# Optimization experiments

Measured on AMD Instinct MI355X. Metric: run time of the kernel, lower is better.

Reference implementation:

```python
import jax, jax.numpy as jnp
import numpy as np
from jax import lax

# --- configuration matching init_kwargs ---
N = 512          # head_size: square cost matrices, marginals a=b=ones(N)
REG = 0.05       # entropy_reg
TAU = 1000.0     # absorption threshold on scaling vectors
N_ITER = 50      # max_iter (fixed iteration count; tol early-exit omitted)
BATCH = 128


def setup_inputs() -> dict:
    key = jax.random.key(0)
    # nonnegative cost matrices, uniform [0,1)
    X = jax.random.uniform(key, (BATCH, N, N), dtype=jnp.float32)
    return {"X": X}


def _sinkhorn_stabilized(M):
    """Log-stabilized Sinkhorn (POT sinkhorn_stabilized) for one cost matrix M [N,N].

    Marginals a = b = ones(N). Returns transport plan Gamma [N,N].
    """
    a = jnp.ones((N,), M.dtype)
    b = jnp.ones((N,), M.dtype)

    def step(carry, _):
        alpha, beta, u, v = carry
        # K = exp(-(M - alpha_i - beta_j)/reg)
        K = jnp.exp((alpha[:, None] + beta[None, :] - M) / REG)
        v = b / (K.T @ u)
        u = a / (K @ v)
        # tau-based absorption of large scalings into the log-domain potentials
        absorb = (jnp.max(jnp.abs(u)) > TAU) | (jnp.max(jnp.abs(v)) > TAU)
        alpha = jnp.where(absorb, alpha + REG * jnp.log(u), alpha)
        beta = jnp.where(absorb, beta + REG * jnp.log(v), beta)
        u = jnp.where(absorb, jnp.full_like(u, 1.0 / N), u)
        v = jnp.where(absorb, jnp.full_like(v, 1.0 / N), v)
        return (alpha, beta, u, v), None

    init = (
        jnp.zeros((N,), M.dtype),          # alpha
        jnp.zeros((N,), M.dtype),          # beta
        jnp.full((N,), 1.0 / N, M.dtype),  # u
        jnp.full((N,), 1.0 / N, M.dtype),  # v
    )
    (alpha, beta, u, v), _ = lax.scan(step, init, None, length=N_ITER)
    # Gamma = exp(-(M - alpha_i - beta_j)/reg + log u_i + log v_j)
    Gamma = jnp.exp(
        (alpha[:, None] + beta[None, :] - M) / REG
        + jnp.log(u)[:, None]
        + jnp.log(v)[None, :]
    )
    return Gamma


def reference(X):
    # original mutates X[i] in place per batch element; we return the batched result
    return jax.vmap(_sinkhorn_stabilized)(X)
```

## Files before the change

kernel.cpp:

```cpp
#include <hip/hip_runtime.h>

constexpr int BN = 512;
constexpr int NITER = 50;

#define CEXP  (-28.853900817779268f)
#define ESH   (14.0f)
#define L2TAU (9.965784284662087f)

typedef unsigned int u32;

__device__ __forceinline__ float fexp2(float x) { return __builtin_amdgcn_exp2f(x); }
__device__ __forceinline__ float flog2(float x) { return __builtin_amdgcn_logf(x); }

__device__ __forceinline__ float nr_rcp(float x) {
    float r = __builtin_amdgcn_rcpf(x);
    return fmaf(r, fmaf(-x, r, 1.0f), r);
}

template <int CTRL>
__device__ __forceinline__ float dppx(float x) {
    return __int_as_float(__builtin_amdgcn_update_dpp(
        0, __float_as_int(x), CTRL, 0xF, 0xF, true));
}

__device__ __forceinline__ float bfly_sum(float x) {
    x += dppx<0xB1>(x);
    x += dppx<0x4E>(x);
    x += dppx<0x141>(x);
    x += dppx<0x140>(x);
    x += __shfl_xor(x, 16, 64);
    x += __shfl_xor(x, 32, 64);
    return x;
}
__device__ __forceinline__ float bfly_max(float x) {
    x = fmaxf(x, dppx<0xB1>(x));
    x = fmaxf(x, dppx<0x4E>(x));
    x = fmaxf(x, dppx<0x141>(x));
    x = fmaxf(x, dppx<0x140>(x));
    x = fmaxf(x, __shfl_xor(x, 16, 64));
    x = fmaxf(x, __shfl_xor(x, 32, 64));
    return x;
}

__device__ __forceinline__ void fma_mix2(float& accLo, float& accHi, u32 e2,
                                         float pLo, float pHi) {
    asm("v_fma_mix_f32 %0, %2, %3, %0 op_sel_hi:[1,0,0]\n\t"
        "v_fma_mix_f32 %1, %2, %4, %1 op_sel:[1,0,0] op_sel_hi:[1,0,0]"
        : "+v"(accLo), "+v"(accHi)
        : "v"(e2), "v"(pLo), "v"(pHi));
}

__device__ __forceinline__ void barrier_lgkm() {
    asm volatile("s_waitcnt lgkmcnt(0)\n\ts_barrier" ::: "memory");
}

__global__ __launch_bounds__(256)
void prep_exp_t(const float* __restrict__ X, float* __restrict__ out)
{
    const int blk  = blockIdx.x;
    const int b    = blk >> 4;
    const int tile = blk & 15;
    const int i0   = (tile >> 2) << 7;
    const int j0   = (tile & 3) << 7;
    const int tid  = threadIdx.x;

    const float* __restrict__ Mb = X + (size_t)b * (BN * BN);
    _Float16* __restrict__ Et = reinterpret_cast<_Float16*>(out + (size_t)b * (BN * BN));

    __shared__ _Float16 T[128][130];

    #pragma unroll
    for (int k = 0; k < 16; ++k) {
        int idx = tid + (k << 8);
        int fi  = idx >> 5;
        int fj  = idx & 31;
        float4 m = *reinterpret_cast<const float4*>(Mb + (size_t)(i0 + fi) * BN + j0 + (fj << 2));
        T[(fj << 2) + 0][fi] = (_Float16)fexp2(fmaf(m.x, CEXP, ESH));
        T[(fj << 2) + 1][fi] = (_Float16)fexp2(fmaf(m.y, CEXP, ESH));
        T[(fj << 2) + 2][fi] = (_Float16)fexp2(fmaf(m.z, CEXP, ESH));
        T[(fj << 2) + 3][fi] = (_Float16)fexp2(fmaf(m.w, CEXP, ESH));
    }
    __syncthreads();
    #pragma unroll
    for (int k = 0; k < 32; ++k) {
        int o  = tid + (k << 8);
        int j  = o >> 6;
        int c2 = o & 63;
        u32 val = *reinterpret_cast<const u32*>(&T[j][c2 << 1]);
        *reinterpret_cast<u32*>(Et + (size_t)(j0 + j) * BN + i0 + (c2 << 1)) = val;
    }
}

__device__ __forceinline__ void consume4(
    uint4 c0, uint4 c1, uint4 c2, uint4 c3, int jb,
    float pr0, float pr1, float pr2, float pr3,
    float pr4, float pr5, float pr6, float pr7,
    float& a0, float& a1, float& a2, float& a3,
    float& a4, float& a5, float& a6, float& a7,
    float& vml, const float* bh, float* lv, int lane)
{
    const float4 bh4 = *reinterpret_cast<const float4*>(&bh[jb]);

    float s00 = 0.f, s01 = 0.f;
    fma_mix2(s00, s01, c0.x, pr0, pr1); fma_mix2(s00, s01, c0.y, pr2, pr3);
    fma_mix2(s00, s01, c0.z, pr4, pr5); fma_mix2(s00, s01, c0.w, pr6, pr7);
    float s10 = 0.f, s11 = 0.f;
    fma_mix2(s10, s11, c1.x, pr0, pr1); fma_mix2(s10, s11, c1.y, pr2, pr3);
    fma_mix2(s10, s11, c1.z, pr4, pr5); fma_mix2(s10, s11, c1.w, pr6, pr7);
    float s20 = 0.f, s21 = 0.f;
    fma_mix2(s20, s21, c2.x, pr0, pr1); fma_mix2(s20, s21, c2.y, pr2, pr3);
    fma_mix2(s20, s21, c2.z, pr4, pr5); fma_mix2(s20, s21, c2.w, pr6, pr7);
    float s30 = 0.f, s31 = 0.f;
    fma_mix2(s30, s31, c3.x, pr0, pr1); fma_mix2(s30, s31, c3.y, pr2, pr3);
    fma_mix2(s30, s31, c3.z, pr4, pr5); fma_mix2(s30, s31, c3.w, pr6, pr7);

    float r0 = bfly_sum(s00 + s01);
    float r1 = bfly_sum(s10 + s11);
    float r2 = bfly_sum(s20 + s21);
    float r3 = bfly_sum(s30 + s31);

    float t0 = r0 * 0x1p-14f, t1 = r1 * 0x1p-14f;
    float t2 = r2 * 0x1p-14f, t3 = r3 * 0x1p-14f;
    float q0 = nr_rcp(t0), q1 = nr_rcp(t1), q2 = nr_rcp(t2), q3 = nr_rcp(t3);
    float l0 = -bh4.x - flog2(t0), l1 = -bh4.y - flog2(t1);
    float l2 = -bh4.z - flog2(t2), l3 = -bh4.w - flog2(t3);
    vml = fmaxf(vml, fmaxf(fmaxf(l0, l1), fmaxf(l2, l3)));
    if (lane == 0)
        *reinterpret_cast<float4*>(&lv[jb]) = make_float4(l0, l1, l2, l3);

    fma_mix2(a0, a1, c0.x, q0, q0); fma_mix2(a2, a3, c0.y, q0, q0);
    fma_mix2(a4, a5, c0.z, q0, q0); fma_mix2(a6, a7, c0.w, q0, q0);
    fma_mix2(a0, a1, c1.x, q1, q1); fma_mix2(a2, a3, c1.y, q1, q1);
    fma_mix2(a4, a5, c1.z, q1, q1); fma_mix2(a6, a7, c1.w, q1, q1);
    fma_mix2(a0, a1, c2.x, q2, q2); fma_mix2(a2, a3, c2.y, q2, q2);
    fma_mix2(a4, a5, c2.z, q2, q2); fma_mix2(a6, a7, c2.w, q2, q2);
    fma_mix2(a0, a1, c3.x, q3, q3); fma_mix2(a2, a3, c3.y, q3, q3);
    fma_mix2(a4, a5, c3.z, q3, q3); fma_mix2(a6, a7, c3.w, q3, q3);
}

__global__ __launch_bounds__(1024)
__attribute__((amdgpu_waves_per_eu(4, 4)))
void sinkhorn_w1024(const float* __restrict__ X, float* __restrict__ out,
                    float* __restrict__ cucv)
{
    const int b    = blockIdx.x;
    const int t    = threadIdx.x;
    const int lane = t & 63;
    const int w    = t >> 6;

    const u32* __restrict__ Et4 =
        reinterpret_cast<const u32*>(out + (size_t)b * (BN * BN));

    __shared__ float ah[BN], bh[BN], lu[BN], lv[BN], pv[BN];
    __shared__ float tpart[8][BN];
    __shared__ float wmaxlu[16], wmaxlv[16];
    __shared__ uint4 stage[16][8][64];

    if (t < BN) {
        ah[t] = 0.f; bh[t] = 0.f;
        lu[t] = -9.f; lv[t] = -9.f;
        pv[t] = 0x1p-9f;
    }

    const int jb0 = w << 5;
    const u32* gbase = Et4 + (size_t)jb0 * 256 + (lane << 2);
#define LD(c) (*reinterpret_cast<const uint4*>(gbase + (size_t)(c) * 256))

    #pragma unroll
    for (int c = 0; c < 8; ++c)
        stage[w][c][lane] = LD(24 + c);

    uint4 e0 = LD(0), e1 = LD(1), e2 = LD(2), e3 = LD(3);
    uint4 f0 = LD(4), f1 = LD(5), f2 = LD(6), f3 = LD(7);
    uint4 h0, h1, h2, h3;

    __syncthreads();

    for (int it = 0; it < NITER; ++it) {
        const float4 prA = *reinterpret_cast<const float4*>(&pv[lane * 8]);
        const float4 prB = *reinterpret_cast<const float4*>(&pv[lane * 8 + 4]);
        const float pr0 = prA.x, pr1 = prA.y, pr2 = prA.z, pr3 = prA.w;
        const float pr4 = prB.x, pr5 = prB.y, pr6 = prB.z, pr7 = prB.w;

        float a0 = 0.f, a1 = 0.f, a2 = 0.f, a3 = 0.f;
        float a4 = 0.f, a5 = 0.f, a6 = 0.f, a7 = 0.f;
        float vml = -1e30f;

#define STEP(B0,B1,B2,B3, I0,I1,I2,I3, ICOL, JOFF)                            \
        I0 = LD((ICOL) + 0); I1 = LD((ICOL) + 1);                             \
        I2 = LD((ICOL) + 2); I3 = LD((ICOL) + 3);                             \
        consume4(B0, B1, B2, B3, jb0 + (JOFF),                                \
                 pr0, pr1, pr2, pr3, pr4, pr5, pr6, pr7,                      \
                 a0, a1, a2, a3, a4, a5, a6, a7, vml, bh, lv, lane);

        STEP(e0,e1,e2,e3, h0,h1,h2,h3,  8,  0)
        STEP(f0,f1,f2,f3, e0,e1,e2,e3, 12,  4)
        STEP(h0,h1,h2,h3, f0,f1,f2,f3, 16,  8)
        STEP(e0,e1,e2,e3, h0,h1,h2,h3, 20, 12)
        STEP(f0,f1,f2,f3, e0,e1,e2,e3,  0, 16)
        STEP(h0,h1,h2,h3, f0,f1,f2,f3,  4, 20)
#undef STEP

        #pragma unroll
        for (int ls = 0; ls < 2; ++ls) {
            uint4 l0v = stage[w][ls * 4 + 0][lane];
            uint4 l1v = stage[w][ls * 4 + 1][lane];
            uint4 l2v = stage[w][ls * 4 + 2][lane];
            uint4 l3v = stage[w][ls * 4 + 3][lane];
            consume4(l0v, l1v, l2v, l3v, jb0 + 24 + ls * 4,
                     pr0, pr1, pr2, pr3, pr4, pr5, pr6, pr7,
                     a0, a1, a2, a3, a4, a5, a6, a7, vml, bh, lv, lane);
        }

        if (w < 8) {
            *reinterpret_cast<float4*>(&tpart[w][lane * 8]) = make_float4(a0, a1, a2, a3);
            *reinterpret_cast<float4*>(&tpart[w][lane * 8 + 4]) = make_float4(a4, a5, a6, a7);
        }
        if (lane == 0) wmaxlv[w] = vml;
        barrier_lgkm();
        if (w >= 8) {
            float4* p0 = reinterpret_cast<float4*>(&tpart[w - 8][lane * 8]);
            float4* p1 = reinterpret_cast<float4*>(&tpart[w - 8][lane * 8 + 4]);
            float4 o0 = *p0, o1 = *p1;
            o0.x += a0; o0.y += a1; o0.z += a2; o0.w += a3;
            o1.x += a4; o1.y += a5; o1.z += a6; o1.w += a7;
            *p0 = o0; *p1 = o1;
        }
        barrier_lgkm();

        float lun = 0.f, tt = 0.f;
        if (t < BN) {
            float p0 = 0, p1 = 0, p2 = 0, p3 = 0;
            #pragma unroll
            for (int w2 = 0; w2 < 8; w2 += 4) {
                p0 += tpart[w2 + 0][t];
                p1 += tpart[w2 + 1][t];
                p2 += tpart[w2 + 2][t];
                p3 += tpart[w2 + 3][t];
            }
            tt  = ((p0 + p1) + (p2 + p3)) * 0x1p-14f;
            lun = -ah[t] - flog2(tt);
            float m = bfly_max(lun);
            if (lane == 0) wmaxlu[w] = m;
        }
        barrier_lgkm();

        if (t < BN) {
            float mlu = wmaxlu[0], mlv = wmaxlv[0];
            #pragma unroll
            for (int i2 = 1; i2 < 8; ++i2)  mlu = fmaxf(mlu, wmaxlu[i2]);
            #pragma unroll
            for (int i2 = 1; i2 < 16; ++i2) mlv = fmaxf(mlv, wmaxlv[i2]);
            if (mlu > L2TAU || mlv > L2TAU) {
                float an = ah[t] + lun;
                ah[t] = an;
                lu[t] = -9.f;
                pv[t] = fexp2(an - 9.0f);
                bh[t] += lv[t];
                lv[t] = -9.f;
            } else {
                lu[t] = lun;
                pv[t] = nr_rcp(tt);
            }
        }
        barrier_lgkm();
    }
#undef LD

    if (t < BN) {
        cucv[(size_t)b * 1024 + t]       = ah[t] + lu[t];
        cucv[(size_t)b * 1024 + 512 + t] = bh[t] + lv[t];
    }
}

__global__ __launch_bounds__(512)
__attribute__((amdgpu_waves_per_eu(2, 2)))
void sinkhorn_w512(const float* __restrict__ X, float* __restrict__ out,
                   float* __restrict__ cucv)
{
    const int b    = blockIdx.x;
    const int t    = threadIdx.x;
    const int lane = t & 63;
    const int w    = t >> 6;

    const u32* __restrict__ Et4 =
        reinterpret_cast<const u32*>(out + (size_t)b * (BN * BN));

    __shared__ float ah[BN], bh[BN], lu[BN], lv[BN], pv[BN];
    __shared__ float tpart[8][BN];
    __shared__ float wmaxlu[8], wmaxlv[8];
    __shared__ uint4 stage[8][16][64];

    ah[t] = 0.f; bh[t] = 0.f;
    lu[t] = -9.f; lv[t] = -9.f;
    pv[t] = 0x1p-9f;

    const int jb0 = w << 6;
    const u32* gbase = Et4 + (size_t)jb0 * 256 + (lane << 2);
#define LD(c) (*reinterpret_cast<const uint4*>(gbase + (size_t)(c) * 256))

    #pragma unroll
    for (int c = 0; c < 16; ++c)
        stage[w][c][lane] = LD(48 + c);

    uint4 e0 = LD(0),  e1 = LD(1),  e2 = LD(2),  e3 = LD(3);
    uint4 f0 = LD(4),  f1 = LD(5),  f2 = LD(6),  f3 = LD(7);
    uint4 h0 = LD(8),  h1 = LD(9),  h2 = LD(10), h3 = LD(11);
    uint4 k0, k1, k2, k3;

    __syncthreads();

    for (int it = 0; it < NITER; ++it) {
        const float4 prA = *reinterpret_cast<const float4*>(&pv[lane * 8]);
        const float4 prB = *reinterpret_cast<const float4*>(&pv[lane * 8 + 4]);
        const float pr0 = prA.x, pr1 = prA.y, pr2 = prA.z, pr3 = prA.w;
        const float pr4 = prB.x, pr5 = prB.y, pr6 = prB.z, pr7 = prB.w;

        float a0 = 0.f, a1 = 0.f, a2 = 0.f, a3 = 0.f;
        float a4 = 0.f, a5 = 0.f, a6 = 0.f, a7 = 0.f;
        float vml = -1e30f;

#define STEP(B0,B1,B2,B3, I0,I1,I2,I3, ICOL, JOFF)                            \
        I0 = LD((ICOL) + 0); I1 = LD((ICOL) + 1);                             \
        I2 = LD((ICOL) + 2); I3 = LD((ICOL) + 3);                             \
        consume4(B0, B1, B2, B3, jb0 + (JOFF),                                \
                 pr0, pr1, pr2, pr3, pr4, pr5, pr6, pr7,                      \
                 a0, a1, a2, a3, a4, a5, a6, a7, vml, bh, lv, lane);

        STEP(e0,e1,e2,e3, k0,k1,k2,k3, 12,  0)
        STEP(f0,f1,f2,f3, e0,e1,e2,e3, 16,  4)
        STEP(h0,h1,h2,h3, f0,f1,f2,f3, 20,  8)
        STEP(k0,k1,k2,k3, h0,h1,h2,h3, 24, 12)
        STEP(e0,e1,e2,e3, k0,k1,k2,k3, 28, 16)
        STEP(f0,f1,f2,f3, e0,e1,e2,e3, 32, 20)
        STEP(h0,h1,h2,h3, f0,f1,f2,f3, 36, 24)
        STEP(k0,k1,k2,k3, h0,h1,h2,h3, 40, 28)
        STEP(e0,e1,e2,e3, k0,k1,k2,k3, 44, 32)
        STEP(f0,f1,f2,f3, e0,e1,e2,e3,  0, 36)
        STEP(h0,h1,h2,h3, f0,f1,f2,f3,  4, 40)
        STEP(k0,k1,k2,k3, h0,h1,h2,h3,  8, 44)
#undef STEP

        #pragma unroll
        for (int ls = 0; ls < 4; ++ls) {
            uint4 l0v = stage[w][ls * 4 + 0][lane];
            uint4 l1v = stage[w][ls * 4 + 1][lane];
            uint4 l2v = stage[w][ls * 4 + 2][lane];
            uint4 l3v = stage[w][ls * 4 + 3][lane];
            consume4(l0v, l1v, l2v, l3v, jb0 + 48 + ls * 4,
                     pr0, pr1, pr2, pr3, pr4, pr5, pr6, pr7,
                     a0, a1, a2, a3, a4, a5, a6, a7, vml, bh, lv, lane);
        }

        *reinterpret_cast<float4*>(&tpart[w][lane * 8]) = make_float4(a0, a1, a2, a3);
        *reinterpret_cast<float4*>(&tpart[w][lane * 8 + 4]) = make_float4(a4, a5, a6, a7);
        if (lane == 0) wmaxlv[w] = vml;
        barrier_lgkm();

        float p0 = 0, p1 = 0, p2 = 0, p3 = 0;
        #pragma unroll
        for (int w2 = 0; w2 < 8; w2 += 4) {
            p0 += tpart[w2 + 0][t];
            p1 += tpart[w2 + 1][t];
            p2 += tpart[w2 + 2][t];
            p3 += tpart[w2 + 3][t];
        }
        float tt  = ((p0 + p1) + (p2 + p3)) * 0x1p-14f;
        float lun = -ah[t] - flog2(tt);
        float m = bfly_max(lun);
        if (lane == 0) wmaxlu[w] = m;
        barrier_lgkm();

        float mlu = wmaxlu[0], mlv = wmaxlv[0];
        #pragma unroll
        for (int i2 = 1; i2 < 8; ++i2) {
            mlu = fmaxf(mlu, wmaxlu[i2]);
            mlv = fmaxf(mlv, wmaxlv[i2]);
        }
        if (mlu > L2TAU || mlv > L2TAU) {
            float an = ah[t] + lun;
            ah[t] = an;
            lu[t] = -9.f;
            pv[t] = fexp2(an - 9.0f);
            bh[t] += lv[t];
            lv[t] = -9.f;
        } else {
            lu[t] = lun;
            pv[t] = nr_rcp(tt);
        }
        barrier_lgkm();
    }
#undef LD

    cucv[(size_t)b * 1024 + t]       = ah[t] + lu[t];
    cucv[(size_t)b * 1024 + 512 + t] = bh[t] + lv[t];
}

__global__ __launch_bounds__(256)
void gamma_out(const float* __restrict__ X, float* __restrict__ out,
               const float* __restrict__ cucv)
{
    const int blk  = blockIdx.x;
    const int b    = blk >> 4;
    const int tile = blk & 15;
    const int tid  = threadIdx.x;
    const int i0   = tile << 5;

    __shared__ float cu[32];
    __shared__ float cv[BN];

    if (tid < 32) cu[tid] = cucv[(size_t)b * 1024 + i0 + tid];
    cv[tid]        = cucv[(size_t)b * 1024 + 512 + tid];
    cv[tid + 256]  = cucv[(size_t)b * 1024 + 768 + tid];
    __syncthreads();

    const float* __restrict__ Mb = X + (size_t)b * (BN * BN);
    float* __restrict__ Gb = out + (size_t)b * (BN * BN);
    const float4* __restrict__ cv4 = reinterpret_cast<const float4*>(cv);

    #pragma unroll
    for (int k = 0; k < 16; ++k) {
        int idx = tid + (k << 8);
        int r   = idx >> 7;
        int c4  = idx & 127;
        int i   = i0 + r;
        float4 m = *reinterpret_cast<const float4*>(Mb + (size_t)i * BN + (c4 << 2));
        float4 c = cv4[c4];
        float cui = cu[r];
        float4 g;
        g.x = fexp2(fmaf(m.x, CEXP, cui + c.x));
        g.y = fexp2(fmaf(m.y, CEXP, cui + c.y));
        g.z = fexp2(fmaf(m.z, CEXP, cui + c.z));
        g.w = fexp2(fmaf(m.w, CEXP, cui + c.w));
        *reinterpret_cast<float4*>(Gb + (size_t)i * BN + (c4 << 2)) = g;
    }
}

extern "C" void kernel_launch(void* const* d_in, const int* in_sizes, int n_in,
                              void* d_out, int out_size, void* d_ws, size_t ws_size,
                              hipStream_t stream)
{
    const float* X = (const float*)d_in[0];
    float* out = (float*)d_out;
    const int batch = in_sizes[0] / (BN * BN);

    prep_exp_t<<<batch * 16, 256, 0, stream>>>(X, out);

    bool w1024_ok = false;
    hipFuncAttributes fa{};
    if (hipFuncGetAttributes(&fa, (const void*)sinkhorn_w1024) == hipSuccess)
        w1024_ok = (fa.localSizeBytes == 0 && fa.numRegs >= 96);

    const size_t cucv_bytes = (size_t)batch * 1024 * sizeof(float);
    if (ws_size >= cucv_bytes) {
        float* cucv = (float*)d_ws;
        if (w1024_ok)
            sinkhorn_w1024<<<batch, 1024, 0, stream>>>(X, out, cucv);
        else
            sinkhorn_w512<<<batch, 512, 0, stream>>>(X, out, cucv);
        gamma_out<<<batch * 16, 256, 0, stream>>>(X, out, cucv);
    } else {
        float* cucv = (float*)d_ws;
        sinkhorn_w512<<<batch, 512, 0, stream>>>(X, out, cucv);
        gamma_out<<<batch * 16, 256, 0, stream>>>(X, out, cucv);
    }
}
```

Measured before the change: 646.7 us.

## Replace log-domain Sinkhorn with scaling-domain v2 kernel using permlane swaps

Adds a new 512-thread Sinkhorn kernel that keeps potentials and scalings in the multiplicative domain, using reciprocals and products instead of per-element log2 and exp2. The tau absorption check becomes a comparison on scaled values, and an extra barrier runs only when absorption fires. Each wave now handles 64 columns with a deeper register/LDS prefetch ring. Cross-half wave reductions use permlane16/32 swap builtins where available instead of shuffles. The 1024-thread kernel is removed. This trades the transcendental work and an extra barrier round for higher register and LDS pressure per wave, and for precision risk from raw rcp without Newton refinement and from the multiplicative potentials.

```diff
diff --git a/kernel.cpp b/kernel.cpp
--- a/kernel.cpp
+++ b/kernel.cpp
@@ -6,14 +6,17 @@
 #define CEXP  (-28.853900817779268f)
 #define ESH   (14.0f)
 #define L2TAU (9.965784284662087f)
+#define TAU_U (1000.0f)
+#define TAU_V (0.06103515625f)
 
 typedef unsigned int u32;
 
 __device__ __forceinline__ float fexp2(float x) { return __builtin_amdgcn_exp2f(x); }
 __device__ __forceinline__ float flog2(float x) { return __builtin_amdgcn_logf(x); }
+__device__ __forceinline__ float frcp(float x)  { return __builtin_amdgcn_rcpf(x); }
 
 __device__ __forceinline__ float nr_rcp(float x) {
-    float r = __builtin_amdgcn_rcpf(x);
+    float r = frcp(x);
     return fmaf(r, fmaf(-x, r, 1.0f), r);
 }
 
@@ -23,7 +26,59 @@
         0, __float_as_int(x), CTRL, 0xF, 0xF, true));
 }
 
+__device__ __forceinline__ float xadd16(float x) {
+#if __has_builtin(__builtin_amdgcn_permlane16_swap)
+    auto r = __builtin_amdgcn_permlane16_swap(__float_as_uint(x), __float_as_uint(x), false, false);
+    return __uint_as_float(r[0]) + __uint_as_float(r[1]);
+#else
+    return x + __shfl_xor(x, 16, 64);
+#endif
+}
+__device__ __forceinline__ float xadd32(float x) {
+#if __has_builtin(__builtin_amdgcn_permlane32_swap)
+    auto r = __builtin_amdgcn_permlane32_swap(__float_as_uint(x), __float_as_uint(x), false, false);
+    return __uint_as_float(r[0]) + __uint_as_float(r[1]);
+#else
+    return x + __shfl_xor(x, 32, 64);
+#endif
+}
+__device__ __forceinline__ float xmax16(float x) {
+#if __has_builtin(__builtin_amdgcn_permlane16_swap)
+    auto r = __builtin_amdgcn_permlane16_swap(__float_as_uint(x), __float_as_uint(x), false, false);
+    return fmaxf(__uint_as_float(r[0]), __uint_as_float(r[1]));
+#else
+    return fmaxf(x, __shfl_xor(x, 16, 64));
+#endif
+}
+__device__ __forceinline__ float xmax32(float x) {
+#if __has_builtin(__builtin_amdgcn_permlane32_swap)
+    auto r = __builtin_amdgcn_permlane32_swap(__float_as_uint(x), __float_as_uint(x), false, false);
+    return fmaxf(__uint_as_float(r[0]), __uint_as_float(r[1]));
+#else
+    return fmaxf(x, __shfl_xor(x, 32, 64));
+#endif
+}
+
 __device__ __forceinline__ float bfly_sum(float x) {
+    x += dppx<0xB1>(x);
+    x += dppx<0x4E>(x);
+    x += dppx<0x141>(x);
+    x += dppx<0x140>(x);
+    x = xadd16(x);
+    x = xadd32(x);
+    return x;
+}
+__device__ __forceinline__ float bfly_max(float x) {
+    x = fmaxf(x, dppx<0xB1>(x));
+    x = fmaxf(x, dppx<0x4E>(x));
+    x = fmaxf(x, dppx<0x141>(x));
+    x = fmaxf(x, dppx<0x140>(x));
+    x = xmax16(x);
+    x = xmax32(x);
+    return x;
+}
+
+__device__ __forceinline__ float bfly_sum_s(float x) {
     x += dppx<0xB1>(x);
     x += dppx<0x4E>(x);
     x += dppx<0x141>(x);
@@ -32,7 +87,7 @@
     x += __shfl_xor(x, 32, 64);
     return x;
 }
-__device__ __forceinline__ float bfly_max(float x) {
+__device__ __forceinline__ float bfly_max_s(float x) {
     x = fmaxf(x, dppx<0xB1>(x));
     x = fmaxf(x, dppx<0x4E>(x));
     x = fmaxf(x, dppx<0x141>(x));
@@ -91,15 +146,15 @@
     }
 }
 
-__device__ __forceinline__ void consume4(
+__device__ __forceinline__ void consume4v2(
     uint4 c0, uint4 c1, uint4 c2, uint4 c3, int jb,
     float pr0, float pr1, float pr2, float pr3,
     float pr4, float pr5, float pr6, float pr7,
     float& a0, float& a1, float& a2, float& a3,
     float& a4, float& a5, float& a6, float& a7,
-    float& vml, const float* bh, float* lv, int lane)
-{
-    const float4 bh4 = *reinterpret_cast<const float4*>(&bh[jb]);
+    float& vml, const float* pbh, float* qv, int lane)
+{
+    const float4 pb4 = *reinterpret_cast<const float4*>(&pbh[jb]);
 
     float s00 = 0.f, s01 = 0.f;
     fma_mix2(s00, s01, c0.x, pr0, pr1); fma_mix2(s00, s01, c0.y, pr2, pr3);
@@ -119,6 +174,172 @@
     float r2 = bfly_sum(s20 + s21);
     float r3 = bfly_sum(s30 + s31);
 
+    float q0 = frcp(r0), q1 = frcp(r1), q2 = frcp(r2), q3 = frcp(r3);
+
+    vml = fmaxf(vml, fmaxf(fmaxf(pb4.x * q0, pb4.y * q1),
+                           fmaxf(pb4.z * q2, pb4.w * q3)));
+    if (lane == 0)
+        *reinterpret_cast<float4*>(&qv[jb]) = make_float4(q0, q1, q2, q3);
+
+    fma_mix2(a0, a1, c0.x, q0, q0); fma_mix2(a2, a3, c0.y, q0, q0);
+    fma_mix2(a4, a5, c0.z, q0, q0); fma_mix2(a6, a7, c0.w, q0, q0);
+    fma_mix2(a0, a1, c1.x, q1, q1); fma_mix2(a2, a3, c1.y, q1, q1);
+    fma_mix2(a4, a5, c1.z, q1, q1); fma_mix2(a6, a7, c1.w, q1, q1);
+    fma_mix2(a0, a1, c2.x, q2, q2); fma_mix2(a2, a3, c2.y, q2, q2);
+    fma_mix2(a4, a5, c2.z, q2, q2); fma_mix2(a6, a7, c2.w, q2, q2);
+    fma_mix2(a0, a1, c3.x, q3, q3); fma_mix2(a2, a3, c3.y, q3, q3);
+    fma_mix2(a4, a5, c3.z, q3, q3); fma_mix2(a6, a7, c3.w, q3, q3);
+}
+
+__global__ __launch_bounds__(512)
+__attribute__((amdgpu_waves_per_eu(2, 2)))
+void sinkhorn_v2(const float* __restrict__ X, float* __restrict__ out,
+                 float* __restrict__ cucv)
+{
+    const int b    = blockIdx.x;
+    const int t    = threadIdx.x;
+    const int lane = t & 63;
+    const int w    = t >> 6;
+
+    const u32* __restrict__ Et4 =
+        reinterpret_cast<const u32*>(out + (size_t)b * (BN * BN));
+
+    __shared__ float pah[BN], pbh[BN], pv[BN], qv[BN];
+    __shared__ float tpart[8][BN];
+    __shared__ float wmaxlu[8], wmaxlv[2][8];
+    __shared__ uint4 stage[8][16][64];
+
+    pah[t] = 1.0f; pbh[t] = 1.0f;
+    pv[t]  = 0x1p-9f; qv[t] = 0x1p-9f;
+
+    const int jb0 = w << 6;
+    const u32* gbase = Et4 + (size_t)jb0 * 256 + (lane << 2);
+#define LD(c) (*reinterpret_cast<const uint4*>(gbase + (size_t)(c) * 256))
+
+    #pragma unroll
+    for (int c = 0; c < 16; ++c)
+        stage[w][c][lane] = LD(48 + c);
+
+    uint4 A0 = LD(0),  A1 = LD(1),  A2 = LD(2),  A3 = LD(3);
+    uint4 B0 = LD(4),  B1 = LD(5),  B2 = LD(6),  B3 = LD(7);
+    uint4 C0 = LD(8),  C1 = LD(9),  C2 = LD(10), C3 = LD(11);
+    uint4 D0 = LD(12), D1 = LD(13), D2 = LD(14), D3 = LD(15);
+    uint4 E0, E1, E2, E3, F0, F1, F2, F3;
+
+    __syncthreads();
+
+    for (int it = 0; it < NITER; ++it) {
+        const float4 prA = *reinterpret_cast<const float4*>(&pv[lane * 8]);
+        const float4 prB = *reinterpret_cast<const float4*>(&pv[lane * 8 + 4]);
+        const float pr0 = prA.x, pr1 = prA.y, pr2 = prA.z, pr3 = prA.w;
+        const float pr4 = prB.x, pr5 = prB.y, pr6 = prB.z, pr7 = prB.w;
+
+        float a0 = 0.f, a1 = 0.f, a2 = 0.f, a3 = 0.f;
+        float a4 = 0.f, a5 = 0.f, a6 = 0.f, a7 = 0.f;
+        float vml = 0.0f;
+
+#define STEP(P0,P1,P2,P3, N0,N1,N2,N3, ICOL, JOFF)                            \
+        N0 = LD((ICOL) + 0); N1 = LD((ICOL) + 1);                             \
+        N2 = LD((ICOL) + 2); N3 = LD((ICOL) + 3);                             \
+        consume4v2(P0, P1, P2, P3, jb0 + (JOFF),                              \
+                   pr0, pr1, pr2, pr3, pr4, pr5, pr6, pr7,                    \
+                   a0, a1, a2, a3, a4, a5, a6, a7, vml, pbh, qv, lane);
+
+        STEP(A0,A1,A2,A3, E0,E1,E2,E3, 16,  0)
+        STEP(B0,B1,B2,B3, F0,F1,F2,F3, 20,  4)
+        STEP(C0,C1,C2,C3, A0,A1,A2,A3, 24,  8)
+        STEP(D0,D1,D2,D3, B0,B1,B2,B3, 28, 12)
+        STEP(E0,E1,E2,E3, C0,C1,C2,C3, 32, 16)
+        STEP(F0,F1,F2,F3, D0,D1,D2,D3, 36, 20)
+        STEP(A0,A1,A2,A3, E0,E1,E2,E3, 40, 24)
+        STEP(B0,B1,B2,B3, F0,F1,F2,F3, 44, 28)
+        STEP(C0,C1,C2,C3, A0,A1,A2,A3,  0, 32)
+        STEP(D0,D1,D2,D3, B0,B1,B2,B3,  4, 36)
+        STEP(E0,E1,E2,E3, C0,C1,C2,C3,  8, 40)
+        STEP(F0,F1,F2,F3, D0,D1,D2,D3, 12, 44)
+#undef STEP
+
+        #pragma unroll
+        for (int ls = 0; ls < 4; ++ls) {
+            uint4 l0v = stage[w][ls * 4 + 0][lane];
+            uint4 l1v = stage[w][ls * 4 + 1][lane];
+            uint4 l2v = stage[w][ls * 4 + 2][lane];
+            uint4 l3v = stage[w][ls * 4 + 3][lane];
+            consume4v2(l0v, l1v, l2v, l3v, jb0 + 48 + ls * 4,
+                       pr0, pr1, pr2, pr3, pr4, pr5, pr6, pr7,
+                       a0, a1, a2, a3, a4, a5, a6, a7, vml, pbh, qv, lane);
+        }
+
+        *reinterpret_cast<float4*>(&tpart[w][lane * 8]) = make_float4(a0, a1, a2, a3);
+        *reinterpret_cast<float4*>(&tpart[w][lane * 8 + 4]) = make_float4(a4, a5, a6, a7);
+        if (lane == 0) wmaxlv[it & 1][w] = vml;
+        barrier_lgkm();
+
+        float p0 = 0, p1 = 0, p2 = 0, p3 = 0;
+        #pragma unroll
+        for (int w2 = 0; w2 < 8; w2 += 4) {
+            p0 += tpart[w2 + 0][t];
+            p1 += tpart[w2 + 1][t];
+            p2 += tpart[w2 + 2][t];
+            p3 += tpart[w2 + 3][t];
+        }
+        float tt  = (p0 + p1) + (p2 + p3);
+        float pvn = frcp(tt);
+        float ul  = pah[t] * pvn;
+        float m   = bfly_max(ul);
+        pv[t] = pvn;
+        if (lane == 0) wmaxlu[w] = m;
+        barrier_lgkm();
+
+        float mlu = wmaxlu[0], mlv = wmaxlv[it & 1][0];
+        #pragma unroll
+        for (int i2 = 1; i2 < 8; ++i2) {
+            mlu = fmaxf(mlu, wmaxlu[i2]);
+            mlv = fmaxf(mlv, wmaxlv[it & 1][i2]);
+        }
+        if (mlu > TAU_U || mlv > TAU_V) {
+            pah[t] = frcp(pvn);
+            pv[t]  = pvn * 0x1p-9f;
+            float qo = qv[t];
+            pbh[t] = 0x1p-14f * frcp(qo);
+            qv[t]  = qo * 0x1p-9f;
+            barrier_lgkm();
+        }
+    }
+#undef LD
+
+    cucv[(size_t)b * 1024 + t]       = flog2(pv[t]);
+    cucv[(size_t)b * 1024 + 512 + t] = 14.0f + flog2(qv[t]);
+}
+
+__device__ __forceinline__ void consume4(
+    uint4 c0, uint4 c1, uint4 c2, uint4 c3, int jb,
+    float pr0, float pr1, float pr2, float pr3,
+    float pr4, float pr5, float pr6, float pr7,
+    float& a0, float& a1, float& a2, float& a3,
+    float& a4, float& a5, float& a6, float& a7,
+    float& vml, const float* bh, float* lv, int lane)
+{
+    const float4 bh4 = *reinterpret_cast<const float4*>(&bh[jb]);
+
+    float s00 = 0.f, s01 = 0.f;
+    fma_mix2(s00, s01, c0.x, pr0, pr1); fma_mix2(s00, s01, c0.y, pr2, pr3);
+    fma_mix2(s00, s01, c0.z, pr4, pr5); fma_mix2(s00, s01, c0.w, pr6, pr7);
+    float s10 = 0.f, s11 = 0.f;
+    fma_mix2(s10, s11, c1.x, pr0, pr1); fma_mix2(s10, s11, c1.y, pr2, pr3);
+    fma_mix2(s10, s11, c1.z, pr4, pr5); fma_mix2(s10, s11, c1.w, pr6, pr7);
+    float s20 = 0.f, s21 = 0.f;
+    fma_mix2(s20, s21, c2.x, pr0, pr1); fma_mix2(s20, s21, c2.y, pr2, pr3);
+    fma_mix2(s20, s21, c2.z, pr4, pr5); fma_mix2(s20, s21, c2.w, pr6, pr7);
+    float s30 = 0.f, s31 = 0.f;
+    fma_mix2(s30, s31, c3.x, pr0, pr1); fma_mix2(s30, s31, c3.y, pr2, pr3);
+    fma_mix2(s30, s31, c3.z, pr4, pr5); fma_mix2(s30, s31, c3.w, pr6, pr7);
+
+    float r0 = bfly_sum_s(s00 + s01);
+    float r1 = bfly_sum_s(s10 + s11);
+    float r2 = bfly_sum_s(s20 + s21);
+    float r3 = bfly_sum_s(s30 + s31);
+
     float t0 = r0 * 0x1p-14f, t1 = r1 * 0x1p-14f;
     float t2 = r2 * 0x1p-14f, t3 = r3 * 0x1p-14f;
     float q0 = nr_rcp(t0), q1 = nr_rcp(t1), q2 = nr_rcp(t2), q3 = nr_rcp(t3);
@@ -136,141 +357,6 @@
     fma_mix2(a4, a5, c2.z, q2, q2); fma_mix2(a6, a7, c2.w, q2, q2);
     fma_mix2(a0, a1, c3.x, q3, q3); fma_mix2(a2, a3, c3.y, q3, q3);
     fma_mix2(a4, a5, c3.z, q3, q3); fma_mix2(a6, a7, c3.w, q3, q3);
-}
-
-__global__ __launch_bounds__(1024)
-__attribute__((amdgpu_waves_per_eu(4, 4)))
-void sinkhorn_w1024(const float* __restrict__ X, float* __restrict__ out,
-                    float* __restrict__ cucv)
-{
-    const int b    = blockIdx.x;
-    const int t    = threadIdx.x;
-    const int lane = t & 63;
-    const int w    = t >> 6;
-
-    const u32* __restrict__ Et4 =
-        reinterpret_cast<const u32*>(out + (size_t)b * (BN * BN));
-
-    __shared__ float ah[BN], bh[BN], lu[BN], lv[BN], pv[BN];
-    __shared__ float tpart[8][BN];
-    __shared__ float wmaxlu[16], wmaxlv[16];
-    __shared__ uint4 stage[16][8][64];
-
-    if (t < BN) {
-        ah[t] = 0.f; bh[t] = 0.f;
-        lu[t] = -9.f; lv[t] = -9.f;
-        pv[t] = 0x1p-9f;
-    }
-
-    const int jb0 = w << 5;
-    const u32* gbase = Et4 + (size_t)jb0 * 256 + (lane << 2);
-#define LD(c) (*reinterpret_cast<const uint4*>(gbase + (size_t)(c) * 256))
-
-    #pragma unroll
-    for (int c = 0; c < 8; ++c)
-        stage[w][c][lane] = LD(24 + c);
-
-    uint4 e0 = LD(0), e1 = LD(1), e2 = LD(2), e3 = LD(3);
-    uint4 f0 = LD(4), f1 = LD(5), f2 = LD(6), f3 = LD(7);
-    uint4 h0, h1, h2, h3;
-
-    __syncthreads();
-
-    for (int it = 0; it < NITER; ++it) {
-        const float4 prA = *reinterpret_cast<const float4*>(&pv[lane * 8]);
-        const float4 prB = *reinterpret_cast<const float4*>(&pv[lane * 8 + 4]);
-        const float pr0 = prA.x, pr1 = prA.y, pr2 = prA.z, pr3 = prA.w;
-        const float pr4 = prB.x, pr5 = prB.y, pr6 = prB.z, pr7 = prB.w;
-
-        float a0 = 0.f, a1 = 0.f, a2 = 0.f, a3 = 0.f;
-        float a4 = 0.f, a5 = 0.f, a6 = 0.f, a7 = 0.f;
-        float vml = -1e30f;
-
-#define STEP(B0,B1,B2,B3, I0,I1,I2,I3, ICOL, JOFF)                            \
-        I0 = LD((ICOL) + 0); I1 = LD((ICOL) + 1);                             \
-        I2 = LD((ICOL) + 2); I3 = LD((ICOL) + 3);                             \
-        consume4(B0, B1, B2, B3, jb0 + (JOFF),                                \
-                 pr0, pr1, pr2, pr3, pr4, pr5, pr6, pr7,                      \
-                 a0, a1, a2, a3, a4, a5, a6, a7, vml, bh, lv, lane);
-
-        STEP(e0,e1,e2,e3, h0,h1,h2,h3,  8,  0)
-        STEP(f0,f1,f2,f3, e0,e1,e2,e3, 12,  4)
-        STEP(h0,h1,h2,h3, f0,f1,f2,f3, 16,  8)
-        STEP(e0,e1,e2,e3, h0,h1,h2,h3, 20, 12)
-        STEP(f0,f1,f2,f3, e0,e1,e2,e3,  0, 16)
-        STEP(h0,h1,h2,h3, f0,f1,f2,f3,  4, 20)
-#undef STEP
-
-        #pragma unroll
-        for (int ls = 0; ls < 2; ++ls) {
-            uint4 l0v = stage[w][ls * 4 + 0][lane];
-            uint4 l1v = stage[w][ls * 4 + 1][lane];
-            uint4 l2v = stage[w][ls * 4 + 2][lane];
-            uint4 l3v = stage[w][ls * 4 + 3][lane];
-            consume4(l0v, l1v, l2v, l3v, jb0 + 24 + ls * 4,
-                     pr0, pr1, pr2, pr3, pr4, pr5, pr6, pr7,
-                     a0, a1, a2, a3, a4, a5, a6, a7, vml, bh, lv, lane);
-        }
-
-        if (w < 8) {
-            *reinterpret_cast<float4*>(&tpart[w][lane * 8]) = make_float4(a0, a1, a2, a3);
-            *reinterpret_cast<float4*>(&tpart[w][lane * 8 + 4]) = make_float4(a4, a5, a6, a7);
-        }
-        if (lane == 0) wmaxlv[w] = vml;
-        barrier_lgkm();
-        if (w >= 8) {
-            float4* p0 = reinterpret_cast<float4*>(&tpart[w - 8][lane * 8]);
-            float4* p1 = reinterpret_cast<float4*>(&tpart[w - 8][lane * 8 + 4]);
-            float4 o0 = *p0, o1 = *p1;
-            o0.x += a0; o0.y += a1; o0.z += a2; o0.w += a3;
-            o1.x += a4; o1.y += a5; o1.z += a6; o1.w += a7;
-            *p0 = o0; *p1 = o1;
-        }
-        barrier_lgkm();
-
-        float lun = 0.f, tt = 0.f;
-        if (t < BN) {
-            float p0 = 0, p1 = 0, p2 = 0, p3 = 0;
-            #pragma unroll
-            for (int w2 = 0; w2 < 8; w2 += 4) {
-                p0 += tpart[w2 + 0][t];
-                p1 += tpart[w2 + 1][t];
-                p2 += tpart[w2 + 2][t];
-                p3 += tpart[w2 + 3][t];
-            }
-            tt  = ((p0 + p1) + (p2 + p3)) * 0x1p-14f;
-            lun = -ah[t] - flog2(tt);
-            float m = bfly_max(lun);
-            if (lane == 0) wmaxlu[w] = m;
-        }
-        barrier_lgkm();
-
-        if (t < BN) {
-            float mlu = wmaxlu[0], mlv = wmaxlv[0];
-            #pragma unroll
-            for (int i2 = 1; i2 < 8; ++i2)  mlu = fmaxf(mlu, wmaxlu[i2]);
-            #pragma unroll
-            for (int i2 = 1; i2 < 16; ++i2) mlv = fmaxf(mlv, wmaxlv[i2]);
-            if (mlu > L2TAU || mlv > L2TAU) {
-                float an = ah[t] + lun;
-                ah[t] = an;
-                lu[t] = -9.f;
-                pv[t] = fexp2(an - 9.0f);
-                bh[t] += lv[t];
-                lv[t] = -9.f;
-            } else {
-                lu[t] = lun;
-                pv[t] = nr_rcp(tt);
-            }
-        }
-        barrier_lgkm();
-    }
-#undef LD
-
-    if (t < BN) {
-        cucv[(size_t)b * 1024 + t]       = ah[t] + lu[t];
-        cucv[(size_t)b * 1024 + 512 + t] = bh[t] + lv[t];
-    }
 }
 
 __global__ __launch_bounds__(512)
@@ -367,7 +453,7 @@
         }
         float tt  = ((p0 + p1) + (p2 + p3)) * 0x1p-14f;
         float lun = -ah[t] - flog2(tt);
-        float m = bfly_max(lun);
+        float m = bfly_max_s(lun);
         if (lane == 0) wmaxlu[w] = m;
         barrier_lgkm();
 
@@ -446,22 +532,15 @@
 
     prep_exp_t<<<batch * 16, 256, 0, stream>>>(X, out);
 
-    bool w1024_ok = false;
+    bool v2_ok = false;
     hipFuncAttributes fa{};
-    if (hipFuncGetAttributes(&fa, (const void*)sinkhorn_w1024) == hipSuccess)
-        w1024_ok = (fa.localSizeBytes == 0 && fa.numRegs >= 96);
-
-    const size_t cucv_bytes = (size_t)batch * 1024 * sizeof(float);
-    if (ws_size >= cucv_bytes) {
-        float* cucv = (float*)d_ws;
-        if (w1024_ok)
-            sinkhorn_w1024<<<batch, 1024, 0, stream>>>(X, out, cucv);
-        else
-            sinkhorn_w512<<<batch, 512, 0, stream>>>(X, out, cucv);
-        gamma_out<<<batch * 16, 256, 0, stream>>>(X, out, cucv);
-    } else {
-        float* cucv = (float*)d_ws;
+    if (hipFuncGetAttributes(&fa, (const void*)sinkhorn_v2) == hipSuccess)
+        v2_ok = (fa.localSizeBytes == 0 && fa.numRegs >= 96);
+
+    float* cucv = (float*)d_ws;
+    if (v2_ok)
+        sinkhorn_v2<<<batch, 512, 0, stream>>>(X, out, cucv);
+    else
         sinkhorn_w512<<<batch, 512, 0, stream>>>(X, out, cucv);
-        gamma_out<<<batch * 16, 256, 0, stream>>>(X, out, cucv);
-    }
-}
+    gamma_out<<<batch * 16, 256, 0, stream>>>(X, out, cucv);
+}
```

New measurement: 644.3 us. About the same (-0.4%).
